# Kernel tuning notes

Hardware: AMD Instinct MI355X
Metric: run time of the kernel (lower is better)

The kernel has to match this reference:

```python
import jax, jax.numpy as jnp
import numpy as np

B, T, IN, H, OUT = 128, 1024, 17, 512, 17


def setup_inputs() -> dict:
    key = jax.random.key(0)
    ks = jax.random.split(key, 11)
    s_in = 1.0 / np.sqrt(H)
    return {
        "x": jax.random.normal(ks[0], (B, T, IN), dtype=jnp.float32),
        "wih0": jax.random.normal(ks[1], (4 * H, IN), dtype=jnp.float32) * s_in,
        "whh0": jax.random.normal(ks[2], (4 * H, H), dtype=jnp.float32) * s_in,
        "bih0": jax.random.normal(ks[3], (4 * H,), dtype=jnp.float32) * s_in,
        "bhh0": jax.random.normal(ks[4], (4 * H,), dtype=jnp.float32) * s_in,
        "wih1": jax.random.normal(ks[5], (4 * H, H), dtype=jnp.float32) * s_in,
        "whh1": jax.random.normal(ks[6], (4 * H, H), dtype=jnp.float32) * s_in,
        "bih1": jax.random.normal(ks[7], (4 * H,), dtype=jnp.float32) * s_in,
        "bhh1": jax.random.normal(ks[8], (4 * H,), dtype=jnp.float32) * s_in,
        "lin_w": jax.random.normal(ks[9], (OUT, H), dtype=jnp.float32) * s_in,
        "lin_b": jax.random.normal(ks[10], (OUT,), dtype=jnp.float32) * s_in,
    }


def _lstm_layer(x, wih, whh, bih, bhh):
    # x: [B, T, D]; gate order i, f, g, o (torch.nn.LSTMCell convention)
    b, _, _ = x.shape
    h = whh.shape[1]
    # Precompute input projection for all timesteps: [B, T, 4H]
    proj = jnp.einsum("btd,gd->btg", x, wih) + bih

    def step(carry, p_t):
        h_t, c_t = carry
        gates = p_t + h_t @ whh.T + bhh  # [B, 4H]
        i, f, g, o = jnp.split(gates, 4, axis=1)
        i = jax.nn.sigmoid(i)
        f = jax.nn.sigmoid(f)
        o = jax.nn.sigmoid(o)
        g = jnp.tanh(g)
        c_t = f * c_t + i * g
        h_t = o * jnp.tanh(c_t)
        return (h_t, c_t), h_t

    h0 = jnp.zeros((b, h), x.dtype)
    c0 = jnp.zeros((b, h), x.dtype)
    _, ys = jax.lax.scan(step, (h0, c0), jnp.swapaxes(proj, 0, 1))  # ys: [T, B, H]
    return jnp.swapaxes(ys, 0, 1)  # [B, T, H]


def reference(x, wih0, whh0, bih0, bhh0, wih1, whh1, bih1, bhh1, lin_w, lin_b):
    y = _lstm_layer(x, wih0, whh0, bih0, bhh0)
    y = _lstm_layer(y, wih1, whh1, bih1, bhh1)
    h_last = y[:, -1, :]  # [B, H]
    return h_last @ lin_w.T + lin_b  # [B, OUT]
```

## Files before the change

### kernel.cpp

```cpp
#include <hip/hip_runtime.h>
#include <cstddef>
#include <cstdint>

typedef unsigned long long ull;
typedef unsigned short u16;
typedef unsigned int u32;
typedef __attribute__((ext_vector_type(8))) short s8v;
typedef __attribute__((ext_vector_type(4))) float f4v;
typedef __attribute__((ext_vector_type(4))) u32 u32x4;

#define GROUPS 8
#define BG     16
#define JS     16
#define TPB    256
#define NT     1024
#define HDIM   512
#define INDIM  17
#define OUTDIM 17
#define BTOT   128

#define AT_LD(p)   __hip_atomic_load((p), __ATOMIC_RELAXED, __HIP_MEMORY_SCOPE_AGENT)
#define AT_ST(p,v) __hip_atomic_store((p), (v), __ATOMIC_RELAXED, __HIP_MEMORY_SCOPE_AGENT)

#define PLANE32 8192
#define WIDX(k, b) ((((k) >> 5) * 512) + ((((k) >> 3) & 3) * 128) + ((b) * 8) + ((k) & 7))

#define RA_OFF     ((size_t)0)
#define RING_BYTES ((size_t)4 * GROUPS * PLANE32 * 4)
#define RB_OFF     (RA_OFF + RING_BYTES)
#define FB32_OFF   (RB_OFF + RING_BYTES)
#define WS_NEEDED  (FB32_OFF + (size_t)BTOT * HDIM * 4)
#define RIX32(sl, gr) (((size_t)(sl) * GROUPS + (gr)) * PLANE32)

#define L_H0   0
#define L_H1   49152
#define L_STG  65536
#define L_CTL  67584
#define LDS_SZ 82944

__device__ __forceinline__ u16 f2bf(float f) {
  unsigned int u = __float_as_uint(f);
  u += 0x7FFFu + ((u >> 16) & 1u);
  return (u16)(u >> 16);
}
__device__ __forceinline__ float bf2f(u16 h) {
  return __uint_as_float(((unsigned int)h) << 16);
}
__device__ __forceinline__ float sigm(float x) { return 1.f / (1.f + __expf(-x)); }
__device__ __forceinline__ float tanh_f(float x) { return 2.f / (1.f + __expf(-2.f * x)) - 1.f; }

#define MFMA(a, b, c) __builtin_amdgcn_mfma_f32_16x16x32_bf16((a), (b), (c), 0, 0, 0)

__device__ __forceinline__ void sc1_read16(const char* base, u32x4 r[16]) {
  asm volatile(
      "global_load_dwordx4 %0, %16, off sc1\n\t"
      "global_load_dwordx4 %1, %16, off offset:1024 sc1\n\t"
      "global_load_dwordx4 %2, %16, off offset:2048 sc1\n\t"
      "global_load_dwordx4 %3, %16, off offset:3072 sc1\n\t"
      "global_load_dwordx4 %4, %17, off sc1\n\t"
      "global_load_dwordx4 %5, %17, off offset:1024 sc1\n\t"
      "global_load_dwordx4 %6, %17, off offset:2048 sc1\n\t"
      "global_load_dwordx4 %7, %17, off offset:3072 sc1\n\t"
      "global_load_dwordx4 %8, %18, off sc1\n\t"
      "global_load_dwordx4 %9, %18, off offset:1024 sc1\n\t"
      "global_load_dwordx4 %10, %18, off offset:2048 sc1\n\t"
      "global_load_dwordx4 %11, %18, off offset:3072 sc1\n\t"
      "global_load_dwordx4 %12, %19, off sc1\n\t"
      "global_load_dwordx4 %13, %19, off offset:1024 sc1\n\t"
      "global_load_dwordx4 %14, %19, off offset:2048 sc1\n\t"
      "global_load_dwordx4 %15, %19, off offset:3072 sc1\n\t"
      "s_waitcnt vmcnt(0)"
      : "=&v"(r[0]), "=&v"(r[1]), "=&v"(r[2]), "=&v"(r[3]),
        "=&v"(r[4]), "=&v"(r[5]), "=&v"(r[6]), "=&v"(r[7]),
        "=&v"(r[8]), "=&v"(r[9]), "=&v"(r[10]), "=&v"(r[11]),
        "=&v"(r[12]), "=&v"(r[13]), "=&v"(r[14]), "=&v"(r[15])
      : "v"(base), "v"(base + 4096), "v"(base + 8192), "v"(base + 12288)
      : "memory");
}

__device__ __forceinline__ void pbar(int* c, int& nbar, int lane) {
  ++nbar;
  if (lane == 0)
    (void)__hip_atomic_fetch_add(c, 1, __ATOMIC_RELEASE, __HIP_MEMORY_SCOPE_WORKGROUP);
  while (__hip_atomic_load(c, __ATOMIC_ACQUIRE, __HIP_MEMORY_SCOPE_WORKGROUP) < 2 * nbar) {}
}

__global__ __launch_bounds__(TPB, 1) void lstm_fused(
    const float* __restrict__ x,
    const float* __restrict__ wih0, const float* __restrict__ whh0,
    const float* __restrict__ bih0, const float* __restrict__ bhh0,
    const float* __restrict__ wih1, const float* __restrict__ whh1,
    const float* __restrict__ bih1, const float* __restrict__ bhh1,
    u32* __restrict__ ringA, u32* __restrict__ ringB,
    float* __restrict__ fb32)
{
  const int bid  = blockIdx.x;
  const int gr   = bid & 7;
  const int wg   = bid >> 3;
  const int j0   = wg * JS;
  const int tid  = threadIdx.x;
  const int wave = tid >> 6;
  const int lane = tid & 63;
  const int n    = lane & 15;
  const int q    = lane >> 4;
  const int k0   = q * 8;
  const int gidx = n & 3;
  const int jl   = n >> 2;

  __shared__ __align__(16) char smem[LDS_SZ];
  int* ctl = (int*)(smem + L_CTL);
  u32* stg = (u32*)(smem + L_STG + (wave & 1) * 512 + (wave >> 1) * 1024);

  if (tid < 16) ctl[tid] = 0;

  {
    int b_l = tid >> 4, j_l = tid & 15, jgw = j0 + j_l;
    int wo = WIDX(jgw, b_l);
    AT_ST(&ringA[RIX32(0, gr) + wo], 0u);
    AT_ST(&ringB[RIX32(0, gr) + wo], 0u);
  }
  __syncthreads();

  const f4v z = {0.f, 0.f, 0.f, 0.f};
  const int half = wave & 1;
  const int pub = (wg >> 1) * 256 + ((wg & 1) * 2 + (wave & 1)) * 64;
  const int sub = (lane >> 2) * 128 + (lane & 3) * 32;
  const ull TMASK = 0xFFFF0000FFFF0000ULL;

  if (wave < 2) {
    int jown[2];
    float bias[2][4];
    s8v wxh[2], wxl[2];
    s8v whh_[2][16], whl_[2][16];
#pragma unroll
    for (int i = 0; i < 2; ++i) {
      const int jc = wave * 2 + i;
      jown[i] = j0 + jc * 4 + q;
      const float* wr = wih0 + (size_t)(gidx * HDIM + j0 + jc * 4 + jl) * INDIM;
#pragma unroll
      for (int j = 0; j < 8; ++j) {
        int k = k0 + j;
        float v = (k < INDIM) ? wr[k] : 0.f;
        u16 hi = f2bf(v);
        wxh[i][j] = (short)hi;
        wxl[i][j] = (short)f2bf(v - bf2f(hi));
      }
      const float* hr = whh0 + (size_t)(gidx * HDIM + j0 + jc * 4 + jl) * HDIM;
#pragma unroll
      for (int kt = 0; kt < 16; ++kt)
#pragma unroll
        for (int j = 0; j < 8; ++j) {
          float v = hr[kt * 32 + k0 + j];
          u16 hi = f2bf(v);
          whh_[i][kt][j] = (short)hi;
          whl_[i][kt][j] = (short)f2bf(v - bf2f(hi));
        }
#pragma unroll
      for (int g = 0; g < 4; ++g)
        bias[i][g] = bih0[g * HDIM + jown[i]] + bhh0[g * HDIM + jown[i]];
    }
    float cc[2] = {0.f, 0.f};
    int nbar = 0;

    for (int s = 1; s <= NT + 1; ++s) {
      f4v xa[2] = {z, z};
      if (s <= NT) {
        const float* xr = x + ((size_t)(gr * BG + n) * NT + (s - 1)) * INDIM;
        s8v bxh, bxl;
#pragma unroll
        for (int j = 0; j < 8; ++j) {
          int k = k0 + j;
          float v = (k < INDIM) ? xr[k] : 0.f;
          u16 hi = f2bf(v);
          bxh[j] = (short)hi;
          bxl[j] = (short)f2bf(v - bf2f(hi));
        }
#pragma unroll
        for (int i = 0; i < 2; ++i) {
          xa[i] = MFMA(wxh[i], bxh, xa[i]);
          xa[i] = MFMA(wxh[i], bxl, xa[i]);
          xa[i] = MFMA(wxl[i], bxh, xa[i]);
        }
      }
      const int sl3 = (s - 1) % 3;
      {
        const char* srcb = (const char*)(ringA + RIX32((s - 1) & 3, gr))
                         + half * 16384;
        const ull tg = (ull)(u16)(s - 1);
        const ull pat = (tg << 16) | (tg << 48);
        const u32 t32 = ((u32)(u16)(s - 1)) << 16;
        for (;;) {
          ull w = AT_LD((const ull*)srcb + sub);
          int l1a = __hip_atomic_load(&ctl[7], __ATOMIC_ACQUIRE,
                                      __HIP_MEMORY_SCOPE_WORKGROUP);
          int l1b = __hip_atomic_load(&ctl[8], __ATOMIC_ACQUIRE,
                                      __HIP_MEMORY_SCOPE_WORKGROUP);
          int l1t = l1a < l1b ? l1a : l1b;
          if (__ballot((((w ^ pat) & TMASK) == 0) & (l1t >= s - 4)) == ~0ULL) break;
          __builtin_amdgcn_s_sleep(1);
        }
        u32x4 r[16];
        for (;;) {
          sc1_read16(srcb + lane * 16, r);
          u32 acc = 0;
#pragma unroll
          for (int i = 0; i < 16; ++i)
#pragma unroll
            for (int jj = 0; jj < 4; ++jj)
              acc |= (r[i][jj] ^ t32) & 0xFFFF0000u;
          if (__ballot(acc == 0) == ~0ULL) break;
          __builtin_amdgcn_s_sleep(1);
        }
        char* dst = smem + L_H0 + sl3 * 16384 + half * 8192;
#pragma unroll
        for (int i = 0; i < 16; ++i) {
          ull packed = (ull)((r[i][0] & 0xFFFFu) | (r[i][1] << 16))
                     | ((ull)((r[i][2] & 0xFFFFu) | (r[i][3] << 16)) << 32);
          *(ull*)(dst + (i * 64 + lane) * 8) = packed;
        }
      }
      pbar(&ctl[0], nbar, lane);
      if (wave == 0 && lane == 0)
        __hip_atomic_store(&ctl[4 + sl3], s - 1, __ATOMIC_RELEASE,
                           __HIP_MEMORY_SCOPE_WORKGROUP);
      if (s == NT + 1) break;

      const char* sh = smem + L_H0 + sl3 * 16384;
      f4v cHH[2] = {z, z}, cHL[2] = {z, z};
#pragma unroll
      for (int kt = 0; kt < 16; ++kt) {
        s8v bh = *(const s8v*)(sh + kt * 1024 + q * 256 + n * 16);
#pragma unroll
        for (int i = 0; i < 2; ++i) {
          cHH[i] = MFMA(whh_[i][kt], bh, cHH[i]);
          cHL[i] = MFMA(whl_[i][kt], bh, cHL[i]);
        }
      }
      const u32 otag = ((u32)(u16)s) << 16;
#pragma unroll
      for (int ii = 0; ii < 2; ++ii) {
        f4v e = xa[ii] + cHH[ii] + cHL[ii];
        float pi = e[0] + bias[ii][0], pf = e[1] + bias[ii][1];
        float pg = e[2] + bias[ii][2], po = e[3] + bias[ii][3];
        float ig = sigm(pi), fg = sigm(pf), gv = tanh_f(pg), og = sigm(po);
        cc[ii] = fg * cc[ii] + ig * gv;
        stg[n * 8 + ii * 4 + q] = otag | (u32)f2bf(og * tanh_f(cc[ii]));
      }
      asm volatile("s_waitcnt lgkmcnt(0)" ::: "memory");
      __builtin_amdgcn_sched_barrier(0);
      if (lane < 32) {
        u32x4 pv = *(const u32x4*)((const char*)stg + lane * 16);
        u32* dp = ringA + RIX32(s & 3, gr) + pub * 2 + lane * 4;
        asm volatile("global_store_dwordx4 %0, %1, off sc1"
                     :: "v"(dp), "v"(pv) : "memory");
      }
    }
  } else {
    int jown[2];
    float bias[2][4];
    s8v w1x_[2][16], w1h_[2][16];
#pragma unroll
    for (int i = 0; i < 2; ++i) {
      const int jc = (wave - 2) * 2 + i;
      jown[i] = j0 + jc * 4 + q;
      const float* p1 = wih1 + (size_t)(gidx * HDIM + j0 + jc * 4 + jl) * HDIM;
      const float* p2 = whh1 + (size_t)(gidx * HDIM + j0 + jc * 4 + jl) * HDIM;
#pragma unroll
      for (int kt = 0; kt < 16; ++kt)
#pragma unroll
        for (int j = 0; j < 8; ++j) {
          w1x_[i][kt][j] = (short)f2bf(p1[kt * 32 + k0 + j]);
          w1h_[i][kt][j] = (short)f2bf(p2[kt * 32 + k0 + j]);
        }
#pragma unroll
      for (int g = 0; g < 4; ++g)
        bias[i][g] = bih1[g * HDIM + jown[i]] + bhh1[g * HDIM + jown[i]];
    }
    float c1[2] = {0.f, 0.f};
    int nbar = 0;

    for (int t = 1; t <= NT; ++t) {
      {
        const char* srcb = (const char*)(ringB + RIX32((t - 1) & 3, gr))
                         + half * 16384;
        const ull tg = (ull)(u16)(t - 1);
        const ull pat = (tg << 16) | (tg << 48);
        const u32 t32 = ((u32)(u16)(t - 1)) << 16;
        for (;;) {
          ull w = AT_LD((const ull*)srcb + sub);
          if (__ballot(((w ^ pat) & TMASK) == 0) == ~0ULL) break;
          __builtin_amdgcn_s_sleep(1);
        }
        u32x4 r[16];
        for (;;) {
          sc1_read16(srcb + lane * 16, r);
          u32 acc = 0;
#pragma unroll
          for (int i = 0; i < 16; ++i)
#pragma unroll
            for (int jj = 0; jj < 4; ++jj)
              acc |= (r[i][jj] ^ t32) & 0xFFFF0000u;
          if (__ballot(acc == 0) == ~0ULL) break;
          __builtin_amdgcn_s_sleep(1);
        }
        char* dst = smem + L_H1 + half * 8192;
#pragma unroll
        for (int i = 0; i < 16; ++i) {
          ull packed = (ull)((r[i][0] & 0xFFFFu) | (r[i][1] << 16))
                     | ((ull)((r[i][2] & 0xFFFFu) | (r[i][3] << 16)) << 32);
          *(ull*)(dst + (i * 64 + lane) * 8) = packed;
        }
      }
      pbar(&ctl[1], nbar, lane);
      const char* th = smem + L_H1;
      f4v dHH[2] = {z, z};
#pragma unroll
      for (int kt = 0; kt < 16; ++kt) {
        s8v bh = *(const s8v*)(th + kt * 1024 + q * 256 + n * 16);
#pragma unroll
        for (int i = 0; i < 2; ++i) dHH[i] = MFMA(w1h_[i][kt], bh, dHH[i]);
      }
      const int sl3 = t % 3;
      while (__hip_atomic_load(&ctl[4 + sl3], __ATOMIC_ACQUIRE,
                               __HIP_MEMORY_SCOPE_WORKGROUP) < t) {}
      const char* sh = smem + L_H0 + sl3 * 16384;
      f4v eHH[2] = {z, z};
#pragma unroll
      for (int kt = 0; kt < 16; ++kt) {
        s8v bh = *(const s8v*)(sh + kt * 1024 + q * 256 + n * 16);
#pragma unroll
        for (int i = 0; i < 2; ++i) eHH[i] = MFMA(w1x_[i][kt], bh, eHH[i]);
      }
      if (lane == 0)
        __hip_atomic_store(&ctl[7 + (wave & 1)], t, __ATOMIC_RELEASE,
                           __HIP_MEMORY_SCOPE_WORKGROUP);
      const u32 otag = ((u32)(u16)t) << 16;
      float hout[2];
#pragma unroll
      for (int ii = 0; ii < 2; ++ii) {
        f4v e = dHH[ii] + eHH[ii];
        float pi = e[0] + bias[ii][0], pf = e[1] + bias[ii][1];
        float pg = e[2] + bias[ii][2], po = e[3] + bias[ii][3];
        float ig = sigm(pi), fg = sigm(pf), gv = tanh_f(pg), og = sigm(po);
        c1[ii] = fg * c1[ii] + ig * gv;
        hout[ii] = og * tanh_f(c1[ii]);
        stg[n * 8 + ii * 4 + q] = otag | (u32)f2bf(hout[ii]);
      }
      asm volatile("s_waitcnt lgkmcnt(0)" ::: "memory");
      __builtin_amdgcn_sched_barrier(0);
      if (lane < 32) {
        u32x4 pv = *(const u32x4*)((const char*)stg + lane * 16);
        u32* dp = ringB + RIX32(t & 3, gr) + pub * 2 + lane * 4;
        asm volatile("global_store_dwordx4 %0, %1, off sc1"
                     :: "v"(dp), "v"(pv) : "memory");
      }
      if (t == NT) {
#pragma unroll
        for (int ii = 0; ii < 2; ++ii)
          AT_ST((u32*)&fb32[(size_t)(gr * BG + n) * HDIM + jown[ii]],
                __float_as_uint(hout[ii]));
      }
    }
  }
}

__global__ void final_linear(const float* __restrict__ fb32,
                             const float* __restrict__ lin_w,
                             const float* __restrict__ lin_b,
                             float* __restrict__ out) {
  int b = blockIdx.x, o = threadIdx.x;
  if (o < OUTDIM) {
    float acc = lin_b[o];
    const u32* hr = (const u32*)(fb32 + (size_t)b * HDIM);
    for (int j = 0; j < HDIM; ++j) {
      float h = __uint_as_float(AT_LD(hr + j));
      acc += h * lin_w[(size_t)o * HDIM + j];
    }
    out[b * OUTDIM + o] = acc;
  }
}

__global__ void sentinel_kernel(float* __restrict__ out, int nv) {
  int i = blockIdx.x * TPB + threadIdx.x;
  if (i < nv) out[i] = 1e30f;
}

extern "C" void kernel_launch(void* const* d_in, const int* in_sizes, int n_in,
                              void* d_out, int out_size, void* d_ws, size_t ws_size,
                              hipStream_t stream) {
  (void)in_sizes; (void)n_in;
  const float* x     = (const float*)d_in[0];
  const float* wih0  = (const float*)d_in[1];
  const float* whh0  = (const float*)d_in[2];
  const float* bih0  = (const float*)d_in[3];
  const float* bhh0  = (const float*)d_in[4];
  const float* wih1  = (const float*)d_in[5];
  const float* whh1  = (const float*)d_in[6];
  const float* bih1  = (const float*)d_in[7];
  const float* bhh1  = (const float*)d_in[8];
  const float* lin_w = (const float*)d_in[9];
  const float* lin_b = (const float*)d_in[10];
  float* out = (float*)d_out;
  char* ws = (char*)d_ws;

  if (ws_size < WS_NEEDED) {
    sentinel_kernel<<<(out_size + TPB - 1) / TPB, TPB, 0, stream>>>(out, out_size);
    return;
  }

  u32* ringA  = (u32*)(ws + RA_OFF);
  u32* ringB  = (u32*)(ws + RB_OFF);
  float* fb32 = (float*)(ws + FB32_OFF);

  lstm_fused<<<256, TPB, 0, stream>>>(x, wih0, whh0, bih0, bhh0,
                                      wih1, whh1, bih1, bhh1,
                                      ringA, ringB, fb32);
  final_linear<<<BTOT, 64, 0, stream>>>(fb32, lin_w, lin_b, out);
}
```

Before: 4.860 ms.

## Add sc0-scoped fast path for cross-workgroup hidden-state ring polling

Polling and bulk reads of the hidden-state ring buffers now first use sc0-scoped loads without sleeping, and fall back to the original sc1 loads with sleep after repeated misses. Producers store each chunk twice, once with sc0 and once with sc1, and ring initialisation also writes through sc0. The goal is lower latency on the per-timestep cross-workgroup exchange, in case neighbouring workgroups share a closer cache level. The cost is extra stores, busier polling, and reliance on cache-coherence behaviour that the tag check and adaptive fallback have to guard.

```diff
diff --git a/kernel.cpp b/kernel.cpp
--- a/kernel.cpp
+++ b/kernel.cpp
@@ -51,31 +51,44 @@
 
 #define MFMA(a, b, c) __builtin_amdgcn_mfma_f32_16x16x32_bf16((a), (b), (c), 0, 0, 0)
 
+__device__ __forceinline__ ull sc0_read8(const ull* p) {
+  ull w;
+  asm volatile("global_load_dwordx2 %0, %1, off sc0\n\ts_waitcnt vmcnt(0)"
+               : "=&v"(w) : "v"(p) : "memory");
+  return w;
+}
+
+#define READ16_BODY(FLAG)                                                  \
+  asm volatile(                                                            \
+      "global_load_dwordx4 %0, %16, off " FLAG "\n\t"                      \
+      "global_load_dwordx4 %1, %16, off offset:1024 " FLAG "\n\t"          \
+      "global_load_dwordx4 %2, %16, off offset:2048 " FLAG "\n\t"          \
+      "global_load_dwordx4 %3, %16, off offset:3072 " FLAG "\n\t"          \
+      "global_load_dwordx4 %4, %17, off " FLAG "\n\t"                      \
+      "global_load_dwordx4 %5, %17, off offset:1024 " FLAG "\n\t"          \
+      "global_load_dwordx4 %6, %17, off offset:2048 " FLAG "\n\t"          \
+      "global_load_dwordx4 %7, %17, off offset:3072 " FLAG "\n\t"          \
+      "global_load_dwordx4 %8, %18, off " FLAG "\n\t"                      \
+      "global_load_dwordx4 %9, %18, off offset:1024 " FLAG "\n\t"          \
+      "global_load_dwordx4 %10, %18, off offset:2048 " FLAG "\n\t"         \
+      "global_load_dwordx4 %11, %18, off offset:3072 " FLAG "\n\t"         \
+      "global_load_dwordx4 %12, %19, off " FLAG "\n\t"                     \
+      "global_load_dwordx4 %13, %19, off offset:1024 " FLAG "\n\t"         \
+      "global_load_dwordx4 %14, %19, off offset:2048 " FLAG "\n\t"         \
+      "global_load_dwordx4 %15, %19, off offset:3072 " FLAG "\n\t"         \
+      "s_waitcnt vmcnt(0)"                                                 \
+      : "=&v"(r[0]), "=&v"(r[1]), "=&v"(r[2]), "=&v"(r[3]),                \
+        "=&v"(r[4]), "=&v"(r[5]), "=&v"(r[6]), "=&v"(r[7]),                \
+        "=&v"(r[8]), "=&v"(r[9]), "=&v"(r[10]), "=&v"(r[11]),              \
+        "=&v"(r[12]), "=&v"(r[13]), "=&v"(r[14]), "=&v"(r[15])             \
+      : "v"(base), "v"(base + 4096), "v"(base + 8192), "v"(base + 12288)   \
+      : "memory")
+
 __device__ __forceinline__ void sc1_read16(const char* base, u32x4 r[16]) {
-  asm volatile(
-      "global_load_dwordx4 %0, %16, off sc1\n\t"
-      "global_load_dwordx4 %1, %16, off offset:1024 sc1\n\t"
-      "global_load_dwordx4 %2, %16, off offset:2048 sc1\n\t"
-      "global_load_dwordx4 %3, %16, off offset:3072 sc1\n\t"
-      "global_load_dwordx4 %4, %17, off sc1\n\t"
-      "global_load_dwordx4 %5, %17, off offset:1024 sc1\n\t"
-      "global_load_dwordx4 %6, %17, off offset:2048 sc1\n\t"
-      "global_load_dwordx4 %7, %17, off offset:3072 sc1\n\t"
-      "global_load_dwordx4 %8, %18, off sc1\n\t"
-      "global_load_dwordx4 %9, %18, off offset:1024 sc1\n\t"
-      "global_load_dwordx4 %10, %18, off offset:2048 sc1\n\t"
-      "global_load_dwordx4 %11, %18, off offset:3072 sc1\n\t"
-      "global_load_dwordx4 %12, %19, off sc1\n\t"
-      "global_load_dwordx4 %13, %19, off offset:1024 sc1\n\t"
-      "global_load_dwordx4 %14, %19, off offset:2048 sc1\n\t"
-      "global_load_dwordx4 %15, %19, off offset:3072 sc1\n\t"
-      "s_waitcnt vmcnt(0)"
-      : "=&v"(r[0]), "=&v"(r[1]), "=&v"(r[2]), "=&v"(r[3]),
-        "=&v"(r[4]), "=&v"(r[5]), "=&v"(r[6]), "=&v"(r[7]),
-        "=&v"(r[8]), "=&v"(r[9]), "=&v"(r[10]), "=&v"(r[11]),
-        "=&v"(r[12]), "=&v"(r[13]), "=&v"(r[14]), "=&v"(r[15])
-      : "v"(base), "v"(base + 4096), "v"(base + 8192), "v"(base + 12288)
-      : "memory");
+  READ16_BODY("sc1");
+}
+__device__ __forceinline__ void sc0_read16(const char* base, u32x4 r[16]) {
+  READ16_BODY("sc0");
 }
 
 __device__ __forceinline__ void pbar(int* c, int& nbar, int lane) {
@@ -116,8 +129,14 @@
   {
     int b_l = tid >> 4, j_l = tid & 15, jgw = j0 + j_l;
     int wo = WIDX(jgw, b_l);
-    AT_ST(&ringA[RIX32(0, gr) + wo], 0u);
-    AT_ST(&ringB[RIX32(0, gr) + wo], 0u);
+    u32* pa = &ringA[RIX32(0, gr) + wo];
+    u32* pb = &ringB[RIX32(0, gr) + wo];
+    u32 zz = 0u;
+    asm volatile("global_store_dword %0, %2, off sc0\n\t"
+                 "global_store_dword %1, %2, off sc0"
+                 :: "v"(pa), "v"(pb), "v"(zz) : "memory");
+    AT_ST(pa, 0u);
+    AT_ST(pb, 0u);
   }
   __syncthreads();
 
@@ -160,7 +179,7 @@
         bias[i][g] = bih0[g * HDIM + jown[i]] + bhh0[g * HDIM + jown[i]];
     }
     float cc[2] = {0.f, 0.f};
-    int nbar = 0;
+    int nbar = 0, fast = 1, miss = 0;
 
     for (int s = 1; s <= NT + 1; ++s) {
       f4v xa[2] = {z, z};
@@ -189,27 +208,49 @@
         const ull tg = (ull)(u16)(s - 1);
         const ull pat = (tg << 16) | (tg << 48);
         const u32 t32 = ((u32)(u16)(s - 1)) << 16;
+        int it = 0;
         for (;;) {
-          ull w = AT_LD((const ull*)srcb + sub);
+          ull w;
+          if (fast && (((++it) & 7) != 0)) w = sc0_read8((const ull*)srcb + sub);
+          else                             w = AT_LD((const ull*)srcb + sub);
           int l1a = __hip_atomic_load(&ctl[7], __ATOMIC_ACQUIRE,
                                       __HIP_MEMORY_SCOPE_WORKGROUP);
           int l1b = __hip_atomic_load(&ctl[8], __ATOMIC_ACQUIRE,
                                       __HIP_MEMORY_SCOPE_WORKGROUP);
           int l1t = l1a < l1b ? l1a : l1b;
           if (__ballot((((w ^ pat) & TMASK) == 0) & (l1t >= s - 4)) == ~0ULL) break;
-          __builtin_amdgcn_s_sleep(1);
+          if (!fast) __builtin_amdgcn_s_sleep(1);
         }
         u32x4 r[16];
-        for (;;) {
-          sc1_read16(srcb + lane * 16, r);
-          u32 acc = 0;
-#pragma unroll
-          for (int i = 0; i < 16; ++i)
-#pragma unroll
-            for (int jj = 0; jj < 4; ++jj)
-              acc |= (r[i][jj] ^ t32) & 0xFFFF0000u;
-          if (__ballot(acc == 0) == ~0ULL) break;
-          __builtin_amdgcn_s_sleep(1);
+        const char* base = srcb + lane * 16;
+        bool got = false;
+        if (fast) {
+#pragma unroll 1
+          for (int att = 0; att < 2 && !got; ++att) {
+            sc0_read16(base, r);
+            u32 acc = 0;
+#pragma unroll
+            for (int i = 0; i < 16; ++i)
+#pragma unroll
+              for (int jj = 0; jj < 4; ++jj)
+                acc |= (r[i][jj] ^ t32) & 0xFFFF0000u;
+            got = (__ballot(acc == 0) == ~0ULL);
+          }
+          miss = got ? 0 : miss + 1;
+          if (miss >= 4) fast = 0;
+        }
+        if (!got) {
+          for (;;) {
+            sc1_read16(base, r);
+            u32 acc = 0;
+#pragma unroll
+            for (int i = 0; i < 16; ++i)
+#pragma unroll
+              for (int jj = 0; jj < 4; ++jj)
+                acc |= (r[i][jj] ^ t32) & 0xFFFF0000u;
+            if (__ballot(acc == 0) == ~0ULL) break;
+            __builtin_amdgcn_s_sleep(1);
+          }
         }
         char* dst = smem + L_H0 + sl3 * 16384 + half * 8192;
 #pragma unroll
@@ -251,7 +292,8 @@
       if (lane < 32) {
         u32x4 pv = *(const u32x4*)((const char*)stg + lane * 16);
         u32* dp = ringA + RIX32(s & 3, gr) + pub * 2 + lane * 4;
-        asm volatile("global_store_dwordx4 %0, %1, off sc1"
+        asm volatile("global_store_dwordx4 %0, %1, off sc0\n\t"
+                     "global_store_dwordx4 %0, %1, off sc1"
                      :: "v"(dp), "v"(pv) : "memory");
       }
     }
@@ -277,7 +319,7 @@
         bias[i][g] = bih1[g * HDIM + jown[i]] + bhh1[g * HDIM + jown[i]];
     }
     float c1[2] = {0.f, 0.f};
-    int nbar = 0;
+    int nbar = 0, fast = 1, miss = 0;
 
     for (int t = 1; t <= NT; ++t) {
       {
@@ -286,22 +328,44 @@
         const ull tg = (ull)(u16)(t - 1);
         const ull pat = (tg << 16) | (tg << 48);
         const u32 t32 = ((u32)(u16)(t - 1)) << 16;
+        int it = 0;
         for (;;) {
-          ull w = AT_LD((const ull*)srcb + sub);
+          ull w;
+          if (fast && (((++it) & 7) != 0)) w = sc0_read8((const ull*)srcb + sub);
+          else                             w = AT_LD((const ull*)srcb + sub);
           if (__ballot(((w ^ pat) & TMASK) == 0) == ~0ULL) break;
-          __builtin_amdgcn_s_sleep(1);
+          if (!fast) __builtin_amdgcn_s_sleep(1);
         }
         u32x4 r[16];
-        for (;;) {
-          sc1_read16(srcb + lane * 16, r);
-          u32 acc = 0;
-#pragma unroll
-          for (int i = 0; i < 16; ++i)
-#pragma unroll
-            for (int jj = 0; jj < 4; ++jj)
-              acc |= (r[i][jj] ^ t32) & 0xFFFF0000u;
-          if (__ballot(acc == 0) == ~0ULL) break;
-          __builtin_amdgcn_s_sleep(1);
+        const char* base = srcb + lane * 16;
+        bool got = false;
+        if (fast) {
+#pragma unroll 1
+          for (int att = 0; att < 2 && !got; ++att) {
+            sc0_read16(base, r);
+            u32 acc = 0;
+#pragma unroll
+            for (int i = 0; i < 16; ++i)
+#pragma unroll
+              for (int jj = 0; jj < 4; ++jj)
+                acc |= (r[i][jj] ^ t32) & 0xFFFF0000u;
+            got = (__ballot(acc == 0) == ~0ULL);
+          }
+          miss = got ? 0 : miss + 1;
+          if (miss >= 4) fast = 0;
+        }
+        if (!got) {
+          for (;;) {
+            sc1_read16(base, r);
+            u32 acc = 0;
+#pragma unroll
+            for (int i = 0; i < 16; ++i)
+#pragma unroll
+              for (int jj = 0; jj < 4; ++jj)
+                acc |= (r[i][jj] ^ t32) & 0xFFFF0000u;
+            if (__ballot(acc == 0) == ~0ULL) break;
+            __builtin_amdgcn_s_sleep(1);
+          }
         }
         char* dst = smem + L_H1 + half * 8192;
 #pragma unroll
@@ -351,7 +415,8 @@
       if (lane < 32) {
         u32x4 pv = *(const u32x4*)((const char*)stg + lane * 16);
         u32* dp = ringB + RIX32(t & 3, gr) + pub * 2 + lane * 4;
-        asm volatile("global_store_dwordx4 %0, %1, off sc1"
+        asm volatile("global_store_dwordx4 %0, %1, off sc0\n\t"
+                     "global_store_dwordx4 %0, %1, off sc1"
                      :: "v"(dp), "v"(pv) : "memory");
       }
       if (t == NT) {
```

Measured after the change: 8.851 ms. 82.1% more time.
